# Kernel optimization log

Hardware: AMD Instinct MI355X
Metric: run time of the kernel (lower is better)

Reference implementation:

```python
import jax, jax.numpy as jnp
import numpy as np

IN_F = 4096
OUT_F = 4096
BATCH = 8192


def setup_inputs() -> dict:
    key = jax.random.key(0)
    ks = jax.random.split(key, 7)
    bound = 1.0 / np.sqrt(IN_F)
    return {
        "x": jax.random.normal(ks[0], (BATCH, IN_F), dtype=jnp.float32),
        "weight_mu": jax.random.normal(ks[1], (OUT_F, IN_F), dtype=jnp.float32) * np.sqrt(2.0 / IN_F),  # kaiming fan_in relu
        "weight_log_var": jnp.full((OUT_F, IN_F), -6.0, dtype=jnp.float32),
        "bias_mu": jax.random.uniform(ks[2], (OUT_F,), dtype=jnp.float32, minval=-bound, maxval=bound),
        "bias_log_var": jnp.full((OUT_F,), -6.0, dtype=jnp.float32),
        "weight_eps": jax.random.normal(ks[3], (OUT_F, IN_F), dtype=jnp.float32),
        "bias_eps": jax.random.normal(ks[4], (OUT_F,), dtype=jnp.float32),
    }


def reference(x, weight_mu, weight_log_var, bias_mu, bias_log_var, weight_eps, bias_eps):
    # Reparameterized sampling: w = mu + eps * exp(0.5 * log_var)
    weight = weight_mu + weight_eps * jnp.exp(0.5 * weight_log_var)   # [out, in]
    bias = bias_mu + bias_eps * jnp.exp(0.5 * bias_log_var)           # [out]
    # F.linear(x, weight, bias) = x @ weight.T + bias
    return jnp.einsum("bi,oi->bo", x, weight) + bias
```

## Files before the change

kernel.cpp:

```cpp
#include <hip/hip_runtime.h>
#include <hip/hip_bf16.h>
#include <stdint.h>

typedef __bf16 bf16x8 __attribute__((ext_vector_type(8)));
typedef float f32x4 __attribute__((ext_vector_type(4)));
typedef unsigned short u16x8 __attribute__((ext_vector_type(8)));

__device__ inline unsigned short f2bf_rne(float f) {
  unsigned int u = __float_as_uint(f);
  u += 0x7fffu + ((u >> 16) & 1u);
  return (unsigned short)(u >> 16);
}

__global__ __launch_bounds__(256) void prep_weight(
    const float4* __restrict__ mu, const float4* __restrict__ lv,
    const float4* __restrict__ eps, u16x8* __restrict__ wbf, int n8) {
  int i = blockIdx.x * 256 + threadIdx.x;
  if (i >= n8) return;
  float4 m0 = mu[2 * i], m1 = mu[2 * i + 1];
  float4 v0 = lv[2 * i], v1 = lv[2 * i + 1];
  float4 e0 = eps[2 * i], e1 = eps[2 * i + 1];
  u16x8 p;
  p[0] = f2bf_rne(m0.x + e0.x * __expf(0.5f * v0.x));
  p[1] = f2bf_rne(m0.y + e0.y * __expf(0.5f * v0.y));
  p[2] = f2bf_rne(m0.z + e0.z * __expf(0.5f * v0.z));
  p[3] = f2bf_rne(m0.w + e0.w * __expf(0.5f * v0.w));
  p[4] = f2bf_rne(m1.x + e1.x * __expf(0.5f * v1.x));
  p[5] = f2bf_rne(m1.y + e1.y * __expf(0.5f * v1.y));
  p[6] = f2bf_rne(m1.z + e1.z * __expf(0.5f * v1.z));
  p[7] = f2bf_rne(m1.w + e1.w * __expf(0.5f * v1.w));
  wbf[i] = p;
}

__global__ __launch_bounds__(256) void prep_x(
    const float4* __restrict__ x, u16x8* __restrict__ xbf, int n8) {
  int i = blockIdx.x * 256 + threadIdx.x;
  if (i >= n8) return;
  float4 m0 = x[2 * i], m1 = x[2 * i + 1];
  u16x8 p;
  p[0] = f2bf_rne(m0.x); p[1] = f2bf_rne(m0.y);
  p[2] = f2bf_rne(m0.z); p[3] = f2bf_rne(m0.w);
  p[4] = f2bf_rne(m1.x); p[5] = f2bf_rne(m1.y);
  p[6] = f2bf_rne(m1.z); p[7] = f2bf_rne(m1.w);
  xbf[i] = p;
}

__global__ __launch_bounds__(512, 2) void gemm_bt_bias(
    const unsigned short* __restrict__ A,
    const unsigned short* __restrict__ B,
    const float* __restrict__ bmu, const float* __restrict__ blv,
    const float* __restrict__ beps,
    float* __restrict__ C, int M, int N, int K) {
  __shared__ __align__(16) unsigned short As[2][2][128 * 64];
  __shared__ __align__(16) unsigned short Bs[2][2][128 * 64];

  const int tid  = threadIdx.x;
  const int wave = tid >> 6;
  const int lane = tid & 63;
  const int wm = wave >> 2;
  const int wn = wave & 3;

  const int rowA0 = blockIdx.y * 256;
  const int rowB0 = blockIdx.x * 256;

  const int srow = tid >> 3;
  const int scol = ((tid & 7) ^ (srow & 7)) * 8;
  const unsigned short* pA = A + (size_t)(rowA0 + srow) * K + scol;
  const unsigned short* pB = B + (size_t)(rowB0 + srow) * K + scol;
  const int dep = wave * 512;

#define GLL(srcp, dstp)                                                     \
  __builtin_amdgcn_global_load_lds(                                         \
      (const __attribute__((address_space(1))) unsigned int*)(srcp),        \
      (__attribute__((address_space(3))) unsigned int*)(dstp), 16, 0, 0)

#define STAGE_A(kt, b, h) do {                                              \
    const unsigned short* s_ = pA + (size_t)((h) * 128) * K + (size_t)(kt) * 64; \
    GLL(s_, &As[b][h][dep]);                                                \
    GLL(s_ + (size_t)64 * K, &As[b][h][4096 + dep]); } while (0)
#define STAGE_B(kt, b, h) do {                                              \
    const unsigned short* s_ = pB + (size_t)((h) * 128) * K + (size_t)(kt) * 64; \
    GLL(s_, &Bs[b][h][dep]);                                                \
    GLL(s_ + (size_t)64 * K, &Bs[b][h][4096 + dep]); } while (0)

  f32x4 acc[8][4];
#pragma unroll
  for (int i = 0; i < 8; ++i)
#pragma unroll
    for (int j = 0; j < 4; ++j)
      acc[i][j] = (f32x4){0.f, 0.f, 0.f, 0.f};

  const int mrow = lane & 15;
  const int gsel = lane >> 4;
  const int pgL = (gsel ^ (mrow & 7)) * 8;
  const int pgH = ((4 + gsel) ^ (mrow & 7)) * 8;
  const int aoff = mrow * 64;
  const int boff = ((wn & 1) * 64 + mrow) * 64;

  STAGE_A(0, 0, 0); STAGE_A(0, 0, 1); STAGE_B(0, 0, 0); STAGE_B(0, 0, 1);
  STAGE_A(1, 1, 0); STAGE_A(1, 1, 1); STAGE_B(1, 1, 0); STAGE_B(1, 1, 1);
  asm volatile("s_waitcnt vmcnt(8)" ::: "memory");
  __builtin_amdgcn_s_barrier();
  __builtin_amdgcn_sched_barrier(0);

  bf16x8 a0[4][2], a1[4][2], b01[2][2], b23[2][2];

  const int NT = K / 64;
  for (int t = 0; t < NT; ++t) {
    const int c = t & 1;
    const unsigned short* as = &As[c][wm][0];
    const unsigned short* bs = &Bs[c][wn >> 1][0];
    const bool pf = (t + 2 < NT);

#pragma unroll
    for (int mi = 0; mi < 4; ++mi) {
      a0[mi][0] = *(const bf16x8*)&as[aoff + mi * 1024 + pgL];
      a0[mi][1] = *(const bf16x8*)&as[aoff + mi * 1024 + pgH];
    }
#pragma unroll
    for (int ni = 0; ni < 2; ++ni) {
      b01[ni][0] = *(const bf16x8*)&bs[boff + ni * 1024 + pgL];
      b01[ni][1] = *(const bf16x8*)&bs[boff + ni * 1024 + pgH];
    }
    __builtin_amdgcn_s_barrier();
    asm volatile("s_waitcnt lgkmcnt(0)" ::: "memory");
    __builtin_amdgcn_sched_barrier(0);
    __builtin_amdgcn_s_setprio(1);
#pragma unroll
    for (int kk = 0; kk < 2; ++kk)
#pragma unroll
      for (int mi = 0; mi < 4; ++mi)
#pragma unroll
        for (int ni = 0; ni < 2; ++ni)
          acc[mi][ni] = __builtin_amdgcn_mfma_f32_16x16x32_bf16(
              a0[mi][kk], b01[ni][kk], acc[mi][ni], 0, 0, 0);
    __builtin_amdgcn_s_setprio(0);
    __builtin_amdgcn_s_barrier();
    __builtin_amdgcn_sched_barrier(0);

#pragma unroll
    for (int mi = 0; mi < 4; ++mi) {
      a1[mi][0] = *(const bf16x8*)&as[aoff + (mi + 4) * 1024 + pgL];
      a1[mi][1] = *(const bf16x8*)&as[aoff + (mi + 4) * 1024 + pgH];
    }
    __builtin_amdgcn_s_barrier();
    asm volatile("s_waitcnt lgkmcnt(0)" ::: "memory");
    __builtin_amdgcn_sched_barrier(0);
    __builtin_amdgcn_s_setprio(1);
#pragma unroll
    for (int kk = 0; kk < 2; ++kk)
#pragma unroll
      for (int mi = 0; mi < 4; ++mi)
#pragma unroll
        for (int ni = 0; ni < 2; ++ni)
          acc[mi + 4][ni] = __builtin_amdgcn_mfma_f32_16x16x32_bf16(
              a1[mi][kk], b01[ni][kk], acc[mi + 4][ni], 0, 0, 0);
    __builtin_amdgcn_s_setprio(0);
    __builtin_amdgcn_s_barrier();
    __builtin_amdgcn_sched_barrier(0);

#pragma unroll
    for (int ni = 0; ni < 2; ++ni) {
      b23[ni][0] = *(const bf16x8*)&bs[boff + (ni + 2) * 1024 + pgL];
      b23[ni][1] = *(const bf16x8*)&bs[boff + (ni + 2) * 1024 + pgH];
    }
    if (pf) { STAGE_A(t + 2, c, 0); STAGE_A(t + 2, c, 1); }
    __builtin_amdgcn_s_barrier();
    asm volatile("s_waitcnt lgkmcnt(0)" ::: "memory");
    __builtin_amdgcn_sched_barrier(0);
    __builtin_amdgcn_s_setprio(1);
#pragma unroll
    for (int kk = 0; kk < 2; ++kk)
#pragma unroll
      for (int mi = 0; mi < 4; ++mi)
#pragma unroll
        for (int ni = 0; ni < 2; ++ni)
          acc[mi + 4][ni + 2] = __builtin_amdgcn_mfma_f32_16x16x32_bf16(
              a1[mi][kk], b23[ni][kk], acc[mi + 4][ni + 2], 0, 0, 0);
    __builtin_amdgcn_s_setprio(0);
    __builtin_amdgcn_s_barrier();
    __builtin_amdgcn_sched_barrier(0);

    if (pf) { STAGE_B(t + 2, c, 0); STAGE_B(t + 2, c, 1); }
    __builtin_amdgcn_s_barrier();
    __builtin_amdgcn_sched_barrier(0);
    __builtin_amdgcn_s_setprio(1);
#pragma unroll
    for (int kk = 0; kk < 2; ++kk)
#pragma unroll
      for (int mi = 0; mi < 4; ++mi)
#pragma unroll
        for (int ni = 0; ni < 2; ++ni)
          acc[mi][ni + 2] = __builtin_amdgcn_mfma_f32_16x16x32_bf16(
              a0[mi][kk], b23[ni][kk], acc[mi][ni + 2], 0, 0, 0);
    __builtin_amdgcn_s_setprio(0);
    if (t + 1 < NT) {
      if (pf) { asm volatile("s_waitcnt vmcnt(8)" ::: "memory"); }
      else    { asm volatile("s_waitcnt vmcnt(0)" ::: "memory"); }
    }
    __builtin_amdgcn_s_barrier();
    __builtin_amdgcn_sched_barrier(0);
  }

  const int colq = lane & 15;
  const int rq4  = (lane >> 4) * 4;
#pragma unroll
  for (int ni = 0; ni < 4; ++ni) {
    const int col = rowB0 + wn * 64 + ni * 16 + colq;
    const float bias = bmu[col] + beps[col] * __expf(0.5f * blv[col]);
#pragma unroll
    for (int mi = 0; mi < 8; ++mi) {
      const int rbase = rowA0 + wm * 128 + mi * 16 + rq4;
#pragma unroll
      for (int r = 0; r < 4; ++r)
        C[(size_t)(rbase + r) * N + col] = acc[mi][ni][r] + bias;
    }
  }
#undef GLL
#undef STAGE_A
#undef STAGE_B
}

extern "C" void kernel_launch(void* const* d_in, const int* in_sizes, int n_in,
                              void* d_out, int out_size, void* d_ws, size_t ws_size,
                              hipStream_t stream) {
  const float* x    = (const float*)d_in[0];
  const float* wmu  = (const float*)d_in[1];
  const float* wlv  = (const float*)d_in[2];
  const float* bmu  = (const float*)d_in[3];
  const float* blv  = (const float*)d_in[4];
  const float* weps = (const float*)d_in[5];
  const float* beps = (const float*)d_in[6];
  float* out = (float*)d_out;

  const int M = 8192, N = 4096, K = 4096;

  unsigned short* xbf = (unsigned short*)d_ws;
  unsigned short* wbf = xbf + (size_t)M * K;

  const int n8w = N * K / 8;
  prep_weight<<<n8w / 256, 256, 0, stream>>>(
      (const float4*)wmu, (const float4*)wlv, (const float4*)weps,
      (u16x8*)wbf, n8w);
  const int n8x = M * K / 8;
  prep_x<<<n8x / 256, 256, 0, stream>>>((const float4*)x, (u16x8*)xbf, n8x);

  dim3 grid(N / 256, M / 256);
  gemm_bt_bias<<<grid, 512, 0, stream>>>(xbf, wbf, bmu, blv, beps, out, M, N, K);
}
```

Before: 631.7 us.

## Software-pipeline LDS fragment loads across MFMA phases with double-buffered registers

Restructures the GEMM main loop so each LDS fragment load is issued before the preceding MFMA batch and overlaps with it, rather than waiting behind a barrier and lgkmcnt drain ahead of the compute. The A0/B01 fragments for the next K-tile are loaded during the last MFMA phase of the current tile, using ping-pong register sets (aX/aY) and a loop manually unrolled by two. This is meant to hide LDS latency behind matrix math. In exchange it raises VGPR pressure from the extra fragment registers and adds tighter ordering between barriers and buffer reuse.

```diff
diff --git a/kernel.cpp b/kernel.cpp
--- a/kernel.cpp
+++ b/kernel.cpp
@@ -97,109 +97,125 @@
   const int aoff = mrow * 64;
   const int boff = ((wn & 1) * 64 + mrow) * 64;
 
+#define BAR() do { __builtin_amdgcn_s_barrier();                            \
+                   __builtin_amdgcn_sched_barrier(0); } while (0)
+#define DRAIN_LGKM() do { asm volatile("s_waitcnt lgkmcnt(0)" ::: "memory");\
+                          __builtin_amdgcn_sched_barrier(0); } while (0)
+
   STAGE_A(0, 0, 0); STAGE_A(0, 0, 1); STAGE_B(0, 0, 0); STAGE_B(0, 0, 1);
   STAGE_A(1, 1, 0); STAGE_A(1, 1, 1); STAGE_B(1, 1, 0); STAGE_B(1, 1, 1);
   asm volatile("s_waitcnt vmcnt(8)" ::: "memory");
-  __builtin_amdgcn_s_barrier();
-  __builtin_amdgcn_sched_barrier(0);
-
-  bf16x8 a0[4][2], a1[4][2], b01[2][2], b23[2][2];
+  BAR();
+
+  bf16x8 aX[4][2], bX01[2][2], aY[4][2], bY01[2][2];
+  bf16x8 a1[4][2], b23[2][2];
+  {
+    const unsigned short* as0 = &As[0][wm][0];
+    const unsigned short* bs0 = &Bs[0][wn >> 1][0];
+#pragma unroll
+    for (int mi = 0; mi < 4; ++mi) {
+      aX[mi][0] = *(const bf16x8*)&as0[aoff + mi * 1024 + pgL];
+      aX[mi][1] = *(const bf16x8*)&as0[aoff + mi * 1024 + pgH];
+    }
+#pragma unroll
+    for (int ni = 0; ni < 2; ++ni) {
+      bX01[ni][0] = *(const bf16x8*)&bs0[boff + ni * 1024 + pgL];
+      bX01[ni][1] = *(const bf16x8*)&bs0[boff + ni * 1024 + pgH];
+    }
+    DRAIN_LGKM();
+  }
 
   const int NT = K / 64;
-  for (int t = 0; t < NT; ++t) {
-    const int c = t & 1;
-    const unsigned short* as = &As[c][wm][0];
-    const unsigned short* bs = &Bs[c][wn >> 1][0];
-    const bool pf = (t + 2 < NT);
-
-#pragma unroll
-    for (int mi = 0; mi < 4; ++mi) {
-      a0[mi][0] = *(const bf16x8*)&as[aoff + mi * 1024 + pgL];
-      a0[mi][1] = *(const bf16x8*)&as[aoff + mi * 1024 + pgH];
-    }
-#pragma unroll
-    for (int ni = 0; ni < 2; ++ni) {
-      b01[ni][0] = *(const bf16x8*)&bs[boff + ni * 1024 + pgL];
-      b01[ni][1] = *(const bf16x8*)&bs[boff + ni * 1024 + pgH];
-    }
-    __builtin_amdgcn_s_barrier();
-    asm volatile("s_waitcnt lgkmcnt(0)" ::: "memory");
-    __builtin_amdgcn_sched_barrier(0);
-    __builtin_amdgcn_s_setprio(1);
-#pragma unroll
-    for (int kk = 0; kk < 2; ++kk)
-#pragma unroll
-      for (int mi = 0; mi < 4; ++mi)
-#pragma unroll
-        for (int ni = 0; ni < 2; ++ni)
-          acc[mi][ni] = __builtin_amdgcn_mfma_f32_16x16x32_bf16(
-              a0[mi][kk], b01[ni][kk], acc[mi][ni], 0, 0, 0);
-    __builtin_amdgcn_s_setprio(0);
-    __builtin_amdgcn_s_barrier();
-    __builtin_amdgcn_sched_barrier(0);
-
-#pragma unroll
-    for (int mi = 0; mi < 4; ++mi) {
-      a1[mi][0] = *(const bf16x8*)&as[aoff + (mi + 4) * 1024 + pgL];
-      a1[mi][1] = *(const bf16x8*)&as[aoff + (mi + 4) * 1024 + pgH];
-    }
-    __builtin_amdgcn_s_barrier();
-    asm volatile("s_waitcnt lgkmcnt(0)" ::: "memory");
-    __builtin_amdgcn_sched_barrier(0);
-    __builtin_amdgcn_s_setprio(1);
-#pragma unroll
-    for (int kk = 0; kk < 2; ++kk)
-#pragma unroll
-      for (int mi = 0; mi < 4; ++mi)
-#pragma unroll
-        for (int ni = 0; ni < 2; ++ni)
-          acc[mi + 4][ni] = __builtin_amdgcn_mfma_f32_16x16x32_bf16(
-              a1[mi][kk], b01[ni][kk], acc[mi + 4][ni], 0, 0, 0);
-    __builtin_amdgcn_s_setprio(0);
-    __builtin_amdgcn_s_barrier();
-    __builtin_amdgcn_sched_barrier(0);
-
-#pragma unroll
-    for (int ni = 0; ni < 2; ++ni) {
-      b23[ni][0] = *(const bf16x8*)&bs[boff + (ni + 2) * 1024 + pgL];
-      b23[ni][1] = *(const bf16x8*)&bs[boff + (ni + 2) * 1024 + pgH];
-    }
-    if (pf) { STAGE_A(t + 2, c, 0); STAGE_A(t + 2, c, 1); }
-    __builtin_amdgcn_s_barrier();
-    asm volatile("s_waitcnt lgkmcnt(0)" ::: "memory");
-    __builtin_amdgcn_sched_barrier(0);
-    __builtin_amdgcn_s_setprio(1);
-#pragma unroll
-    for (int kk = 0; kk < 2; ++kk)
-#pragma unroll
-      for (int mi = 0; mi < 4; ++mi)
-#pragma unroll
-        for (int ni = 0; ni < 2; ++ni)
-          acc[mi + 4][ni + 2] = __builtin_amdgcn_mfma_f32_16x16x32_bf16(
-              a1[mi][kk], b23[ni][kk], acc[mi + 4][ni + 2], 0, 0, 0);
-    __builtin_amdgcn_s_setprio(0);
-    __builtin_amdgcn_s_barrier();
-    __builtin_amdgcn_sched_barrier(0);
-
-    if (pf) { STAGE_B(t + 2, c, 0); STAGE_B(t + 2, c, 1); }
-    __builtin_amdgcn_s_barrier();
-    __builtin_amdgcn_sched_barrier(0);
-    __builtin_amdgcn_s_setprio(1);
-#pragma unroll
-    for (int kk = 0; kk < 2; ++kk)
-#pragma unroll
-      for (int mi = 0; mi < 4; ++mi)
-#pragma unroll
-        for (int ni = 0; ni < 2; ++ni)
-          acc[mi][ni + 2] = __builtin_amdgcn_mfma_f32_16x16x32_bf16(
-              a0[mi][kk], b23[ni][kk], acc[mi][ni + 2], 0, 0, 0);
-    __builtin_amdgcn_s_setprio(0);
-    if (t + 1 < NT) {
-      if (pf) { asm volatile("s_waitcnt vmcnt(8)" ::: "memory"); }
-      else    { asm volatile("s_waitcnt vmcnt(0)" ::: "memory"); }
-    }
-    __builtin_amdgcn_s_barrier();
-    __builtin_amdgcn_sched_barrier(0);
+
+#define TILE(T, CB, NB, A0, B01, A0N, B01N) do {                              \
+    const unsigned short* as_  = &As[CB][wm][0];                              \
+    const unsigned short* bs_  = &Bs[CB][wn >> 1][0];                         \
+    const unsigned short* asn_ = &As[NB][wm][0];                              \
+    const unsigned short* bsn_ = &Bs[NB][wn >> 1][0];                         \
+    const bool pf = ((T) + 2 < NT);                                           \
+    const bool pr = ((T) + 1 < NT);                                           \
+                                             \
+    _Pragma("unroll")                                                         \
+    for (int mi = 0; mi < 4; ++mi) {                                          \
+      a1[mi][0] = *(const bf16x8*)&as_[aoff + (mi + 4) * 1024 + pgL];         \
+      a1[mi][1] = *(const bf16x8*)&as_[aoff + (mi + 4) * 1024 + pgH];         \
+    }                                                                         \
+    __builtin_amdgcn_s_setprio(1);                                            \
+    _Pragma("unroll")                                                         \
+    for (int kk = 0; kk < 2; ++kk)                                            \
+      _Pragma("unroll")                                                       \
+      for (int mi = 0; mi < 4; ++mi)                                          \
+        _Pragma("unroll")                                                     \
+        for (int ni = 0; ni < 2; ++ni)                                        \
+          acc[mi][ni] = __builtin_amdgcn_mfma_f32_16x16x32_bf16(              \
+              A0[mi][kk], B01[ni][kk], acc[mi][ni], 0, 0, 0);                 \
+    __builtin_amdgcn_s_setprio(0);                                            \
+    DRAIN_LGKM(); BAR();                                                      \
+                             \
+    _Pragma("unroll")                                                         \
+    for (int ni = 0; ni < 2; ++ni) {                                          \
+      b23[ni][0] = *(const bf16x8*)&bs_[boff + (ni + 2) * 1024 + pgL];        \
+      b23[ni][1] = *(const bf16x8*)&bs_[boff + (ni + 2) * 1024 + pgH];        \
+    }                                                                         \
+    if (pf) { STAGE_A((T) + 2, CB, 0); STAGE_A((T) + 2, CB, 1); }             \
+    __builtin_amdgcn_s_setprio(1);                                            \
+    _Pragma("unroll")                                                         \
+    for (int kk = 0; kk < 2; ++kk)                                            \
+      _Pragma("unroll")                                                       \
+      for (int mi = 0; mi < 4; ++mi)                                          \
+        _Pragma("unroll")                                                     \
+        for (int ni = 0; ni < 2; ++ni)                                        \
+          acc[mi + 4][ni] = __builtin_amdgcn_mfma_f32_16x16x32_bf16(          \
+              a1[mi][kk], B01[ni][kk], acc[mi + 4][ni], 0, 0, 0);             \
+    __builtin_amdgcn_s_setprio(0);                                            \
+    DRAIN_LGKM(); BAR();                                                      \
+               \
+    if (pf) { STAGE_B((T) + 2, CB, 0); STAGE_B((T) + 2, CB, 1); }             \
+    __builtin_amdgcn_s_setprio(1);                                            \
+    _Pragma("unroll")                                                         \
+    for (int kk = 0; kk < 2; ++kk)                                            \
+      _Pragma("unroll")                                                       \
+      for (int mi = 0; mi < 4; ++mi)                                          \
+        _Pragma("unroll")                                                     \
+        for (int ni = 0; ni < 2; ++ni)                                        \
+          acc[mi + 4][ni + 2] = __builtin_amdgcn_mfma_f32_16x16x32_bf16(      \
+              a1[mi][kk], b23[ni][kk], acc[mi + 4][ni + 2], 0, 0, 0);         \
+    __builtin_amdgcn_s_setprio(0);                                            \
+    if (pr) {                                                                 \
+      if (pf) { asm volatile("s_waitcnt vmcnt(8)" ::: "memory"); }            \
+      else    { asm volatile("s_waitcnt vmcnt(0)" ::: "memory"); }            \
+      __builtin_amdgcn_sched_barrier(0);                                      \
+    }                                                                         \
+    BAR();                                                                    \
+           \
+    if (pr) {                                                                 \
+      _Pragma("unroll")                                                       \
+      for (int mi = 0; mi < 4; ++mi) {                                        \
+        A0N[mi][0] = *(const bf16x8*)&asn_[aoff + mi * 1024 + pgL];           \
+        A0N[mi][1] = *(const bf16x8*)&asn_[aoff + mi * 1024 + pgH];           \
+      }                                                                       \
+      _Pragma("unroll")                                                       \
+      for (int ni = 0; ni < 2; ++ni) {                                        \
+        B01N[ni][0] = *(const bf16x8*)&bsn_[boff + ni * 1024 + pgL];          \
+        B01N[ni][1] = *(const bf16x8*)&bsn_[boff + ni * 1024 + pgH];          \
+      }                                                                       \
+    }                                                                         \
+    __builtin_amdgcn_s_setprio(1);                                            \
+    _Pragma("unroll")                                                         \
+    for (int kk = 0; kk < 2; ++kk)                                            \
+      _Pragma("unroll")                                                       \
+      for (int mi = 0; mi < 4; ++mi)                                          \
+        _Pragma("unroll")                                                     \
+        for (int ni = 0; ni < 2; ++ni)                                        \
+          acc[mi][ni + 2] = __builtin_amdgcn_mfma_f32_16x16x32_bf16(          \
+              A0[mi][kk], b23[ni][kk], acc[mi][ni + 2], 0, 0, 0);             \
+    __builtin_amdgcn_s_setprio(0);                                            \
+    DRAIN_LGKM(); BAR();                                                      \
+  } while (0)
+
+  for (int t = 0; t < NT; t += 2) {
+    TILE(t,     0, 1, aX, bX01, aY, bY01);
+    TILE(t + 1, 1, 0, aY, bY01, aX, bX01);
   }
 
   const int colq = lane & 15;
@@ -219,6 +235,9 @@
 #undef GLL
 #undef STAGE_A
 #undef STAGE_B
+#undef BAR
+#undef DRAIN_LGKM
+#undef TILE
 }
 
 extern "C" void kernel_launch(void* const* d_in, const int* in_sizes, int n_in,
```

Result: slower. 1.789 ms (+183.2%).

## Collapse per-phase barriers into two barriers per K-tile in GEMM main loop

Applied to the files above, without the earlier changes.

Restructures the bf16 MFMA main loop so all A and B fragment LDS reads for the tile are issued up front, and the four compute phases run without intermediate workgroup barriers. Only one LDS wait plus barrier before the prefetch of tile t+2 into the same buffer and one barrier at the end of the iteration remain. The aim is to cut barrier stalls and let the compiler overlap LDS reads with MFMAs. The cost is more live fragment registers and less explicit interleaving between waves.

```diff
diff --git a/kernel.cpp b/kernel.cpp
--- a/kernel.cpp
+++ b/kernel.cpp
@@ -108,66 +108,65 @@
   const int NT = K / 64;
   for (int t = 0; t < NT; ++t) {
     const int c = t & 1;
-    const unsigned short* as = &As[c][wm][0];
-    const unsigned short* bs = &Bs[c][wn >> 1][0];
+    const unsigned short* as_ = &As[c][wm][0];
+    const unsigned short* bs_ = &Bs[c][wn >> 1][0];
     const bool pf = (t + 2 < NT);
+    const bool pr = (t + 1 < NT);
 
 #pragma unroll
     for (int mi = 0; mi < 4; ++mi) {
-      a0[mi][0] = *(const bf16x8*)&as[aoff + mi * 1024 + pgL];
-      a0[mi][1] = *(const bf16x8*)&as[aoff + mi * 1024 + pgH];
+      a0[mi][0] = *(const bf16x8*)&as_[aoff + mi * 1024 + pgL];
+      a0[mi][1] = *(const bf16x8*)&as_[aoff + mi * 1024 + pgH];
     }
 #pragma unroll
     for (int ni = 0; ni < 2; ++ni) {
-      b01[ni][0] = *(const bf16x8*)&bs[boff + ni * 1024 + pgL];
-      b01[ni][1] = *(const bf16x8*)&bs[boff + ni * 1024 + pgH];
-    }
-    __builtin_amdgcn_s_barrier();
+      b01[ni][0] = *(const bf16x8*)&bs_[boff + ni * 1024 + pgL];
+      b01[ni][1] = *(const bf16x8*)&bs_[boff + ni * 1024 + pgH];
+    }
+#pragma unroll
+    for (int mi = 0; mi < 4; ++mi) {
+      a1[mi][0] = *(const bf16x8*)&as_[aoff + (mi + 4) * 1024 + pgL];
+      a1[mi][1] = *(const bf16x8*)&as_[aoff + (mi + 4) * 1024 + pgH];
+    }
+
+    __builtin_amdgcn_s_setprio(1);
+#pragma unroll
+    for (int kk = 0; kk < 2; ++kk)
+#pragma unroll
+      for (int mi = 0; mi < 4; ++mi)
+#pragma unroll
+        for (int ni = 0; ni < 2; ++ni)
+          acc[mi][ni] = __builtin_amdgcn_mfma_f32_16x16x32_bf16(
+              a0[mi][kk], b01[ni][kk], acc[mi][ni], 0, 0, 0);
+    __builtin_amdgcn_s_setprio(0);
+
+#pragma unroll
+    for (int ni = 0; ni < 2; ++ni) {
+      b23[ni][0] = *(const bf16x8*)&bs_[boff + (ni + 2) * 1024 + pgL];
+      b23[ni][1] = *(const bf16x8*)&bs_[boff + (ni + 2) * 1024 + pgH];
+    }
+
+    __builtin_amdgcn_s_setprio(1);
+#pragma unroll
+    for (int kk = 0; kk < 2; ++kk)
+#pragma unroll
+      for (int mi = 0; mi < 4; ++mi)
+#pragma unroll
+        for (int ni = 0; ni < 2; ++ni)
+          acc[mi + 4][ni] = __builtin_amdgcn_mfma_f32_16x16x32_bf16(
+              a1[mi][kk], b01[ni][kk], acc[mi + 4][ni], 0, 0, 0);
+    __builtin_amdgcn_s_setprio(0);
+
     asm volatile("s_waitcnt lgkmcnt(0)" ::: "memory");
     __builtin_amdgcn_sched_barrier(0);
-    __builtin_amdgcn_s_setprio(1);
-#pragma unroll
-    for (int kk = 0; kk < 2; ++kk)
-#pragma unroll
-      for (int mi = 0; mi < 4; ++mi)
-#pragma unroll
-        for (int ni = 0; ni < 2; ++ni)
-          acc[mi][ni] = __builtin_amdgcn_mfma_f32_16x16x32_bf16(
-              a0[mi][kk], b01[ni][kk], acc[mi][ni], 0, 0, 0);
-    __builtin_amdgcn_s_setprio(0);
     __builtin_amdgcn_s_barrier();
     __builtin_amdgcn_sched_barrier(0);
 
-#pragma unroll
-    for (int mi = 0; mi < 4; ++mi) {
-      a1[mi][0] = *(const bf16x8*)&as[aoff + (mi + 4) * 1024 + pgL];
-      a1[mi][1] = *(const bf16x8*)&as[aoff + (mi + 4) * 1024 + pgH];
-    }
-    __builtin_amdgcn_s_barrier();
-    asm volatile("s_waitcnt lgkmcnt(0)" ::: "memory");
-    __builtin_amdgcn_sched_barrier(0);
-    __builtin_amdgcn_s_setprio(1);
-#pragma unroll
-    for (int kk = 0; kk < 2; ++kk)
-#pragma unroll
-      for (int mi = 0; mi < 4; ++mi)
-#pragma unroll
-        for (int ni = 0; ni < 2; ++ni)
-          acc[mi + 4][ni] = __builtin_amdgcn_mfma_f32_16x16x32_bf16(
-              a1[mi][kk], b01[ni][kk], acc[mi + 4][ni], 0, 0, 0);
-    __builtin_amdgcn_s_setprio(0);
-    __builtin_amdgcn_s_barrier();
-    __builtin_amdgcn_sched_barrier(0);
-
-#pragma unroll
-    for (int ni = 0; ni < 2; ++ni) {
-      b23[ni][0] = *(const bf16x8*)&bs[boff + (ni + 2) * 1024 + pgL];
-      b23[ni][1] = *(const bf16x8*)&bs[boff + (ni + 2) * 1024 + pgH];
-    }
-    if (pf) { STAGE_A(t + 2, c, 0); STAGE_A(t + 2, c, 1); }
-    __builtin_amdgcn_s_barrier();
-    asm volatile("s_waitcnt lgkmcnt(0)" ::: "memory");
-    __builtin_amdgcn_sched_barrier(0);
+    if (pf) {
+      STAGE_A(t + 2, c, 0); STAGE_A(t + 2, c, 1);
+      STAGE_B(t + 2, c, 0); STAGE_B(t + 2, c, 1);
+    }
+
     __builtin_amdgcn_s_setprio(1);
 #pragma unroll
     for (int kk = 0; kk < 2; ++kk)
@@ -178,12 +177,7 @@
           acc[mi + 4][ni + 2] = __builtin_amdgcn_mfma_f32_16x16x32_bf16(
               a1[mi][kk], b23[ni][kk], acc[mi + 4][ni + 2], 0, 0, 0);
     __builtin_amdgcn_s_setprio(0);
-    __builtin_amdgcn_s_barrier();
-    __builtin_amdgcn_sched_barrier(0);
-
-    if (pf) { STAGE_B(t + 2, c, 0); STAGE_B(t + 2, c, 1); }
-    __builtin_amdgcn_s_barrier();
-    __builtin_amdgcn_sched_barrier(0);
+
     __builtin_amdgcn_s_setprio(1);
 #pragma unroll
     for (int kk = 0; kk < 2; ++kk)
@@ -194,12 +188,14 @@
           acc[mi][ni + 2] = __builtin_amdgcn_mfma_f32_16x16x32_bf16(
               a0[mi][kk], b23[ni][kk], acc[mi][ni + 2], 0, 0, 0);
     __builtin_amdgcn_s_setprio(0);
-    if (t + 1 < NT) {
+
+    if (pr) {
       if (pf) { asm volatile("s_waitcnt vmcnt(8)" ::: "memory"); }
       else    { asm volatile("s_waitcnt vmcnt(0)" ::: "memory"); }
-    }
-    __builtin_amdgcn_s_barrier();
-    __builtin_amdgcn_sched_barrier(0);
+      __builtin_amdgcn_sched_barrier(0);
+      __builtin_amdgcn_s_barrier();
+      __builtin_amdgcn_sched_barrier(0);
+    }
   }
 
   const int colq = lane & 15;
```

New measurement: 603.6 us. 4.5% less time.
